# Performance work log

Measured on AMD Instinct MI355X. Metric: run time of the kernel, lower is better.

## Reference

```python
import jax, jax.numpy as jnp
import numpy as np
from jax import lax

ROUTE_SCALE = 1.0
TOPK = 2


def conv2d(x, w, stride=1, pad=1):
    # x: [B, Cin, H, W], w: [Cout, Cin, kh, kw]
    return lax.conv_general_dilated(
        x, w, window_strides=(stride, stride),
        padding=[(pad, pad), (pad, pad)],
        dimension_numbers=("NCHW", "OIHW", "NCHW"))


def setup_inputs() -> dict:
    key = jax.random.key(0)
    ks = jax.random.split(key, 6)
    B, Cin, Cout, H, W, E = 8, 32, 32, 256, 256, 8
    x = jax.random.normal(ks[0], (B, Cin, H, W), dtype=jnp.float32)
    gate_w = jax.random.normal(ks[1], (E, Cin, 3, 3), dtype=jnp.float32) * 0.05
    gate_bias = jnp.zeros((E,), dtype=jnp.float32)  # load-balance bias buffer (zero in eval)
    expert_w = jax.random.normal(ks[2], (E, Cout, Cin, 3, 3), dtype=jnp.float32) * 0.05
    expert_b = jax.random.normal(ks[3], (E, Cout), dtype=jnp.float32) * 0.05
    shared_w = jax.random.normal(ks[4], (Cout, Cin, 3, 3), dtype=jnp.float32) * 0.05
    shared_b = jax.random.normal(ks[5], (Cout,), dtype=jnp.float32) * 0.05
    return {"x": x, "gate_w": gate_w, "gate_bias": gate_bias,
            "expert_w": expert_w, "expert_b": expert_b,
            "shared_w": shared_w, "shared_b": shared_b}


def reference(x, gate_w, gate_bias, expert_w, expert_b, shared_w, shared_b):
    B, Cin, H, W = x.shape
    E, Cout = expert_w.shape[0], expert_w.shape[1]
    # ---- Gate: sigmoid(conv) -> per-pixel top-k over expert channel dim ----
    scores = jax.nn.sigmoid(conv2d(x, gate_w))                 # [B, E, H, W]
    biased = scores + gate_bias[None, :, None, None]
    st = jnp.moveaxis(scores, 1, -1)                            # [B, H, W, E]
    bt = jnp.moveaxis(biased, 1, -1)
    _, idx = lax.top_k(bt, TOPK)                                # [B, H, W, K]
    w = jnp.take_along_axis(st, idx, axis=-1)                   # gather raw scores
    w = jax.nn.softmax(w, axis=-1) * ROUTE_SCALE                # [B, H, W, K]
    # dense per-expert routing weight: sum_k w_k * onehot(idx_k)
    onehot = jax.nn.one_hot(idx, E, dtype=x.dtype)              # [B, H, W, K, E]
    dense = jnp.einsum('bhwk,bhwke->bhwe', w, onehot)           # [B, H, W, E]
    dense = jnp.moveaxis(dense, -1, 1)                          # [B, E, H, W]
    # ---- All expert convs as one stacked conv, masked accumulate ----
    ew = expert_w.reshape(E * Cout, Cin, 3, 3)
    eo = conv2d(x, ew) + expert_b.reshape(-1)[None, :, None, None]
    eo = eo.reshape(B, E, Cout, H, W)
    out = jnp.einsum('bechw,behw->bchw', eo, dense)
    # ---- Shared expert ----
    out = out + conv2d(x, shared_w) + shared_b[None, :, None, None]
    return out
```

## Files before the change

kernel.cpp:

```cpp
#include <hip/hip_runtime.h>

typedef __attribute__((ext_vector_type(8)))  short bf16x8;
typedef __attribute__((ext_vector_type(16))) float f32x16;

#define XIM (32*256*256)

__device__ __forceinline__ short f2bf(float f){
    unsigned int u = __builtin_bit_cast(unsigned int, f);
    u += 0x7fffu + ((u >> 16) & 1u);
    return (short)(u >> 16);
}
__device__ __forceinline__ float bf2f(short s){
    unsigned int u = ((unsigned int)(unsigned short)s) << 16;
    return __builtin_bit_cast(float, u);
}
__device__ __forceinline__ void glds16(const short* g, short* l){
    __builtin_amdgcn_global_load_lds(
        (const __attribute__((address_space(1))) unsigned int*)g,
        (__attribute__((address_space(3))) unsigned int*)l,
        16, 0, 0);
}

__global__ __launch_bounds__(256) void prep_weights(const float* __restrict__ ew,
                                                    const float* __restrict__ sw,
                                                    const float* __restrict__ ebv,
                                                    const float* __restrict__ sbv,
                                                    short* __restrict__ wt2){
    int i = blockIdx.x * 256 + threadIdx.x;
    if(i < 73728){
        int c7  = i & 7;
        int col = (i >> 3) & 31;
        int cio = (i >> 8) & 3;
        int rest = i >> 10;
        int tap = rest % 9;
        int es  = rest / 9;
        int ci  = cio*8 + c7;
        float v = ew[((es*32 + col)*32 + ci)*9 + tap] + sw[(col*32 + ci)*9 + tap];
        wt2[i] = f2bf(v);
    } else {
        int j = i - 73728, c = j >> 4, k = j & 15;
        float v = (k < 8) ? (ebv[k*32 + c] + sbv[c]) : 0.f;
        wt2[i] = f2bf(v);
    }
}

__global__ __launch_bounds__(256) void gate_kernel(const float* __restrict__ x,
                                                   const float* __restrict__ gw,
                                                   const float* __restrict__ gb,
                                                   short* __restrict__ route){
    __shared__ float xs[2][16][272];
    int raw = blockIdx.x;
    int wg  = (raw & 7)*128 + (raw >> 3);
    int b   = wg >> 7;
    int y0  = (wg & 127) * 2;
    int t   = threadIdx.x;
    int wv  = t >> 6, lane = t & 63;
    const float* xim = x + (size_t)b * XIM;

    if(t < 64){
        int bufi = t >> 5, s2 = (t >> 1) & 15;
        if(t & 1) xs[bufi][s2][260] = 0.f; else xs[bufi][s2][3] = 0.f;
    }

    float4 ld[4];
    auto LOAD = [&](int cc){
        #pragma unroll
        for(int sg=0; sg<4; ++sg){
            int seg = wv*4 + sg;
            int r4  = seg >> 2, cid = seg & 3;
            int ci  = cc*4 + cid;
            int yy  = y0 - 1 + r4;
            float4 v = make_float4(0.f,0.f,0.f,0.f);
            if(yy >= 0 && yy < 256)
                v = *(const float4*)(xim + ((size_t)ci*256 + yy)*256 + lane*4);
            ld[sg] = v;
        }
    };
    auto WRITE = [&](int bufi){
        #pragma unroll
        for(int sg=0; sg<4; ++sg){
            int seg = wv*4 + sg;
            *(float4*)(&xs[bufi][seg][4 + lane*4]) = ld[sg];
        }
    };

    float g[2][8];
    #pragma unroll
    for(int pr=0;pr<2;++pr)
        #pragma unroll
        for(int e=0;e<8;++e) g[pr][e] = 0.f;

    LOAD(0); WRITE(0);
    __syncthreads();
    for(int cc=0; cc<8; ++cc){
        if(cc < 7) LOAD(cc+1);
        const int bufi = cc & 1;
        #pragma unroll
        for(int cid=0; cid<4; ++cid){
            float sv[4][3];
            #pragma unroll
            for(int r4=0;r4<4;++r4){
                sv[r4][0] = xs[bufi][r4*4+cid][t+3];
                sv[r4][1] = xs[bufi][r4*4+cid][t+4];
                sv[r4][2] = xs[bufi][r4*4+cid][t+5];
            }
            const float* gwp = gw + (cc*4 + cid)*9;
            #pragma unroll
            for(int e=0;e<8;++e){
                #pragma unroll
                for(int kh=0;kh<3;++kh){
                    #pragma unroll
                    for(int kw=0;kw<3;++kw){
                        float wval = gwp[e*288 + kh*3 + kw];
                        g[0][e] = fmaf(sv[kh][kw],   wval, g[0][e]);
                        g[1][e] = fmaf(sv[kh+1][kw], wval, g[1][e]);
                    }
                }
            }
        }
        if(cc < 7) WRITE((cc+1)&1);
        __syncthreads();
    }

    #pragma unroll
    for(int pr=0; pr<2; ++pr){
        float v1b=-1e30f, v2b=-1e30f, v3b=-1e30f, r1=0.f, r2=0.f; int i1=-1, i2=-1;
        #pragma unroll
        for(int e=0;e<8;e++){
            float se = 1.f/(1.f + expf(-g[pr][e]));
            float be = se + gb[e];
            if(be > v1b){ v3b=v2b; v2b=v1b; r2=r1; i2=i1; v1b=be; r1=se; i1=e; }
            else if(be > v2b){ v3b=v2b; v2b=be; r2=se; i2=e; }
            else if(be > v3b){ v3b=be; }
        }
        if(v2b - v3b < 2e-5f){
            int y = y0 + pr;
            double gd[8];
            #pragma unroll
            for(int e=0;e<8;e++) gd[e] = 0.0;
            for(int ci=0; ci<32; ++ci){
                for(int kh=0; kh<3; ++kh){
                    int yy = y + kh - 1;
                    if(yy < 0 || yy >= 256) continue;
                    const float* xr = xim + ((size_t)ci*256 + yy)*256;
                    for(int kw=0; kw<3; ++kw){
                        int xx = t + kw - 1;
                        if(xx < 0 || xx >= 256) continue;
                        double xv = (double)xr[xx];
                        const float* gwp = gw + ci*9 + kh*3 + kw;
                        #pragma unroll
                        for(int e=0;e<8;e++) gd[e] += xv * (double)gwp[e*288];
                    }
                }
            }
            double b1=-1e30, b2=-1e30; double rr1=0.0, rr2=0.0; int j1=-1, j2=-1;
            #pragma unroll
            for(int e=0;e<8;e++){
                double sd = 1.0/(1.0 + exp(-gd[e]));
                double bd = sd + (double)gb[e];
                if(bd > b1){ b2=b1; rr2=rr1; j2=j1; b1=bd; rr1=sd; j1=e; }
                else if(bd > b2){ b2=bd; rr2=sd; j2=e; }
            }
            i1=j1; i2=j2; r1=(float)rr1; r2=(float)rr2;
        }
        float m  = fmaxf(r1, r2);
        float e1 = expf(r1-m), e2 = expf(r2-m);
        float inv = 1.f/(e1+e2);
        float w1 = e1*inv, w2 = e2*inv;
        bf16x8 ov;
        #pragma unroll
        for(int e=0;e<8;e++){
            float dv = (e==i1) ? w1 : ((e==i2) ? w2 : 0.f);
            ov[e] = f2bf(dv);
        }
        *(bf16x8*)(route + ((size_t)(b*256 + y0 + pr)*256 + t)*8) = ov;
    }
}

__global__ __launch_bounds__(512, 2) void moe_main(const float* __restrict__ x,
                                                   const short* __restrict__ wt2,
                                                   const short* __restrict__ route,
                                                   float* __restrict__ out){
    __shared__ __align__(16) short wlds[73728];
    __shared__ __align__(16) short xt[10*2*34*8];
    int raw = blockIdx.x;
    int wg  = (raw & 7)*256 + (raw >> 3);
    int b   = wg >> 8;
    int y0  = ((wg >> 3) & 31) * 8;
    int x0  = (wg & 7) * 32;
    int t   = threadIdx.x;
    int wv  = t >> 6, l = t & 63, col = l & 31, hi = l >> 5;

    #pragma unroll
    for(int j=0;j<18;++j){
        int c = wv + 8*j;
        glds16(wt2 + c*512 + l*8, wlds + c*512);
    }

    const float* xim = x + (size_t)b*XIM;
    int yy = y0 + wv;
    bf16x8 biasA = *(const bf16x8*)(wt2 + 73728 + col*16 + hi*8);
    bf16x8 rfrag = *(const bf16x8*)(route + ((size_t)(b*256 + yy)*256 + x0 + col)*8);

    bf16x8 Bf[3][2][3];
    #pragma unroll
    for(int hf=0; hf<2; ++hf){
        if(hf) __syncthreads();
        #pragma unroll
        for(int i=0;i<2;++i){
            int u = t + i*512;
            if(u < 640){
                int px = u & 31, rc = u >> 5;
                int row = rc >> 1, cic = rc & 1;
                int cib = hf*16 + cic*8;
                int ry = y0 - 1 + row, xx = x0 - 1 + px;
                bool ok = (ry>=0 && ry<256 && xx>=0 && xx<256);
                bf16x8 pk;
                #pragma unroll
                for(int j2=0;j2<8;++j2){
                    float v = ok ? xim[((size_t)(cib+j2)*256 + ry)*256 + xx] : 0.f;
                    pk[j2] = f2bf(v);
                }
                *(bf16x8*)(&xt[((row*2 + cic)*34 + px)*8]) = pk;
            }
        }
        if(t < 40){
            int pxh = 32 + (t & 1), rc = t >> 1;
            int row = rc >> 1, cic = rc & 1;
            int cib = hf*16 + cic*8;
            int ry = y0 - 1 + row, xx = x0 - 1 + pxh;
            bool ok = (ry>=0 && ry<256 && xx>=0 && xx<256);
            bf16x8 pk;
            #pragma unroll
            for(int j2=0;j2<8;++j2){
                float v = ok ? xim[((size_t)(cib+j2)*256 + ry)*256 + xx] : 0.f;
                pk[j2] = f2bf(v);
            }
            *(bf16x8*)(&xt[((row*2 + cic)*34 + pxh)*8]) = pk;
        }
        __syncthreads();
        #pragma unroll
        for(int kh=0;kh<3;++kh)
            #pragma unroll
            for(int kw=0;kw<3;++kw)
                Bf[kh][hf][kw] = *(const bf16x8*)(&xt[(((wv+kh)*2 + hi)*34 + col + kw)*8]);
    }

    f32x16 z = {};
    f32x16 oa = __builtin_amdgcn_mfma_f32_32x32x16_bf16(biasA, rfrag, z, 0,0,0);

    #pragma unroll
    for(int es=0; es<8; ++es){
        f32x16 acc = {};
        #pragma unroll
        for(int tap=0; tap<9; ++tap){
            const int kh = tap/3, kw = tap - kh*3;
            #pragma unroll
            for(int hf=0; hf<2; ++hf){
                bf16x8 a = *(const bf16x8*)(&wlds[(((es*9 + tap)*4 + hf*2 + hi)*32 + col)*8]);
                acc = __builtin_amdgcn_mfma_f32_32x32x16_bf16(a, Bf[kh][hf][kw], acc, 0,0,0);
            }
        }
        float d = bf2f(rfrag[es]);
        #pragma unroll
        for(int r=0;r<16;r++) oa[r] += d*acc[r];
    }

    float* ob = out + (size_t)b*XIM;
    #pragma unroll
    for(int r=0;r<16;r++){
        int c = hi*4 + (r&3) + 8*(r>>2);
        ob[((size_t)c*256 + yy)*256 + x0 + col] = oa[r];
    }
}

extern "C" void kernel_launch(void* const* d_in, const int* in_sizes, int n_in,
                              void* d_out, int out_size, void* d_ws, size_t ws_size,
                              hipStream_t stream){
    (void)in_sizes; (void)n_in; (void)out_size; (void)ws_size;
    const float* x   = (const float*)d_in[0];
    const float* gw  = (const float*)d_in[1];
    const float* gb  = (const float*)d_in[2];
    const float* ew  = (const float*)d_in[3];
    const float* ebv = (const float*)d_in[4];
    const float* sw  = (const float*)d_in[5];
    const float* sbv = (const float*)d_in[6];
    float* out = (float*)d_out;

    short* route = (short*)d_ws;
    short* wt2   = route + (size_t)8*256*256*8;

    prep_weights<<<dim3(290),  dim3(256), 0, stream>>>(ew, sw, ebv, sbv, wt2);
    gate_kernel <<<dim3(1024), dim3(256), 0, stream>>>(x, gw, gb, route);
    moe_main    <<<dim3(2048), dim3(512), 0, stream>>>(x, wt2, route, out);
}
```

Before: 220.2 us.

## Fuse gate conv into main MFMA kernel with fp16 and exact-route fixup pass

Removes the separate fp32 gate kernel and its route buffer. The gate conv now runs as extra fp16 MFMAs inside the main kernel, reusing the already-staged input tiles. All MFMAs switch from bf16 to fp16 for more mantissa precision. Pixels whose top-2 margin is ambiguous are appended to an atomic list, and two new kernels recompute their routing in double precision and rewrite their outputs in fp32. This trades a full gate pass and route traffic for an atomic counter, extra gate MFMAs, two small serial fixup kernels, and a hard cap on how many pixels can be fixed.

```diff
diff --git a/kernel.cpp b/kernel.cpp
--- a/kernel.cpp
+++ b/kernel.cpp
@@ -1,18 +1,14 @@
 #include <hip/hip_runtime.h>
 
-typedef __attribute__((ext_vector_type(8)))  short bf16x8;
+typedef __attribute__((ext_vector_type(8)))  _Float16 f16x8;
 typedef __attribute__((ext_vector_type(16))) float f32x16;
 
 #define XIM (32*256*256)
-
-__device__ __forceinline__ short f2bf(float f){
-    unsigned int u = __builtin_bit_cast(unsigned int, f);
-    u += 0x7fffu + ((u >> 16) & 1u);
-    return (short)(u >> 16);
-}
-__device__ __forceinline__ float bf2f(short s){
-    unsigned int u = ((unsigned int)(unsigned short)s) << 16;
-    return __builtin_bit_cast(float, u);
+#define MAXFIX 32768
+
+__device__ __forceinline__ short f2h(float f){
+    _Float16 h = (_Float16)f;
+    return __builtin_bit_cast(short, h);
 }
 __device__ __forceinline__ void glds16(const short* g, short* l){
     __builtin_amdgcn_global_load_lds(
@@ -25,8 +21,12 @@
                                                     const float* __restrict__ sw,
                                                     const float* __restrict__ ebv,
                                                     const float* __restrict__ sbv,
-                                                    short* __restrict__ wt2){
+                                                    const float* __restrict__ gw,
+                                                    short* __restrict__ wt2,
+                                                    short* __restrict__ gwA,
+                                                    int* __restrict__ cnt){
     int i = blockIdx.x * 256 + threadIdx.x;
+    if(i == 0) *cnt = 0;
     if(i < 73728){
         int c7  = i & 7;
         int col = (i >> 3) & 31;
@@ -36,151 +36,29 @@
         int es  = rest / 9;
         int ci  = cio*8 + c7;
         float v = ew[((es*32 + col)*32 + ci)*9 + tap] + sw[(col*32 + ci)*9 + tap];
-        wt2[i] = f2bf(v);
-    } else {
+        wt2[i] = f2h(v);
+    } else if(i < 74240){
         int j = i - 73728, c = j >> 4, k = j & 15;
         float v = (k < 8) ? (ebv[k*32 + c] + sbv[c]) : 0.f;
-        wt2[i] = f2bf(v);
-    }
-}
-
-__global__ __launch_bounds__(256) void gate_kernel(const float* __restrict__ x,
-                                                   const float* __restrict__ gw,
-                                                   const float* __restrict__ gb,
-                                                   short* __restrict__ route){
-    __shared__ float xs[2][16][272];
-    int raw = blockIdx.x;
-    int wg  = (raw & 7)*128 + (raw >> 3);
-    int b   = wg >> 7;
-    int y0  = (wg & 127) * 2;
-    int t   = threadIdx.x;
-    int wv  = t >> 6, lane = t & 63;
-    const float* xim = x + (size_t)b * XIM;
-
-    if(t < 64){
-        int bufi = t >> 5, s2 = (t >> 1) & 15;
-        if(t & 1) xs[bufi][s2][260] = 0.f; else xs[bufi][s2][3] = 0.f;
-    }
-
-    float4 ld[4];
-    auto LOAD = [&](int cc){
-        #pragma unroll
-        for(int sg=0; sg<4; ++sg){
-            int seg = wv*4 + sg;
-            int r4  = seg >> 2, cid = seg & 3;
-            int ci  = cc*4 + cid;
-            int yy  = y0 - 1 + r4;
-            float4 v = make_float4(0.f,0.f,0.f,0.f);
-            if(yy >= 0 && yy < 256)
-                v = *(const float4*)(xim + ((size_t)ci*256 + yy)*256 + lane*4);
-            ld[sg] = v;
-        }
-    };
-    auto WRITE = [&](int bufi){
-        #pragma unroll
-        for(int sg=0; sg<4; ++sg){
-            int seg = wv*4 + sg;
-            *(float4*)(&xs[bufi][seg][4 + lane*4]) = ld[sg];
-        }
-    };
-
-    float g[2][8];
-    #pragma unroll
-    for(int pr=0;pr<2;++pr)
-        #pragma unroll
-        for(int e=0;e<8;++e) g[pr][e] = 0.f;
-
-    LOAD(0); WRITE(0);
-    __syncthreads();
-    for(int cc=0; cc<8; ++cc){
-        if(cc < 7) LOAD(cc+1);
-        const int bufi = cc & 1;
-        #pragma unroll
-        for(int cid=0; cid<4; ++cid){
-            float sv[4][3];
-            #pragma unroll
-            for(int r4=0;r4<4;++r4){
-                sv[r4][0] = xs[bufi][r4*4+cid][t+3];
-                sv[r4][1] = xs[bufi][r4*4+cid][t+4];
-                sv[r4][2] = xs[bufi][r4*4+cid][t+5];
-            }
-            const float* gwp = gw + (cc*4 + cid)*9;
-            #pragma unroll
-            for(int e=0;e<8;++e){
-                #pragma unroll
-                for(int kh=0;kh<3;++kh){
-                    #pragma unroll
-                    for(int kw=0;kw<3;++kw){
-                        float wval = gwp[e*288 + kh*3 + kw];
-                        g[0][e] = fmaf(sv[kh][kw],   wval, g[0][e]);
-                        g[1][e] = fmaf(sv[kh+1][kw], wval, g[1][e]);
-                    }
-                }
-            }
-        }
-        if(cc < 7) WRITE((cc+1)&1);
-        __syncthreads();
-    }
-
-    #pragma unroll
-    for(int pr=0; pr<2; ++pr){
-        float v1b=-1e30f, v2b=-1e30f, v3b=-1e30f, r1=0.f, r2=0.f; int i1=-1, i2=-1;
-        #pragma unroll
-        for(int e=0;e<8;e++){
-            float se = 1.f/(1.f + expf(-g[pr][e]));
-            float be = se + gb[e];
-            if(be > v1b){ v3b=v2b; v2b=v1b; r2=r1; i2=i1; v1b=be; r1=se; i1=e; }
-            else if(be > v2b){ v3b=v2b; v2b=be; r2=se; i2=e; }
-            else if(be > v3b){ v3b=be; }
-        }
-        if(v2b - v3b < 2e-5f){
-            int y = y0 + pr;
-            double gd[8];
-            #pragma unroll
-            for(int e=0;e<8;e++) gd[e] = 0.0;
-            for(int ci=0; ci<32; ++ci){
-                for(int kh=0; kh<3; ++kh){
-                    int yy = y + kh - 1;
-                    if(yy < 0 || yy >= 256) continue;
-                    const float* xr = xim + ((size_t)ci*256 + yy)*256;
-                    for(int kw=0; kw<3; ++kw){
-                        int xx = t + kw - 1;
-                        if(xx < 0 || xx >= 256) continue;
-                        double xv = (double)xr[xx];
-                        const float* gwp = gw + ci*9 + kh*3 + kw;
-                        #pragma unroll
-                        for(int e=0;e<8;e++) gd[e] += xv * (double)gwp[e*288];
-                    }
-                }
-            }
-            double b1=-1e30, b2=-1e30; double rr1=0.0, rr2=0.0; int j1=-1, j2=-1;
-            #pragma unroll
-            for(int e=0;e<8;e++){
-                double sd = 1.0/(1.0 + exp(-gd[e]));
-                double bd = sd + (double)gb[e];
-                if(bd > b1){ b2=b1; rr2=rr1; j2=j1; b1=bd; rr1=sd; j1=e; }
-                else if(bd > b2){ b2=bd; rr2=sd; j2=e; }
-            }
-            i1=j1; i2=j2; r1=(float)rr1; r2=(float)rr2;
-        }
-        float m  = fmaxf(r1, r2);
-        float e1 = expf(r1-m), e2 = expf(r2-m);
-        float inv = 1.f/(e1+e2);
-        float w1 = e1*inv, w2 = e2*inv;
-        bf16x8 ov;
-        #pragma unroll
-        for(int e=0;e<8;e++){
-            float dv = (e==i1) ? w1 : ((e==i2) ? w2 : 0.f);
-            ov[e] = f2bf(dv);
-        }
-        *(bf16x8*)(route + ((size_t)(b*256 + y0 + pr)*256 + t)*8) = ov;
+        wt2[i] = f2h(v);
+    } else {
+        int i2 = i - 74240;
+        int c7  = i2 & 7;
+        int row = (i2 >> 3) & 31;
+        int cio = (i2 >> 8) & 3;
+        int tap = i2 >> 10;
+        float v = (row < 8) ? gw[row*288 + (cio*8 + c7)*9 + tap] : 0.f;
+        gwA[i2] = f2h(v);
     }
 }
 
 __global__ __launch_bounds__(512, 2) void moe_main(const float* __restrict__ x,
                                                    const short* __restrict__ wt2,
-                                                   const short* __restrict__ route,
-                                                   float* __restrict__ out){
+                                                   const short* __restrict__ gwA,
+                                                   const float* __restrict__ gb,
+                                                   float* __restrict__ out,
+                                                   int* __restrict__ cnt,
+                                                   int* __restrict__ fixlist){
     __shared__ __align__(16) short wlds[73728];
     __shared__ __align__(16) short xt[10*2*34*8];
     int raw = blockIdx.x;
@@ -199,10 +77,9 @@
 
     const float* xim = x + (size_t)b*XIM;
     int yy = y0 + wv;
-    bf16x8 biasA = *(const bf16x8*)(wt2 + 73728 + col*16 + hi*8);
-    bf16x8 rfrag = *(const bf16x8*)(route + ((size_t)(b*256 + yy)*256 + x0 + col)*8);
-
-    bf16x8 Bf[3][2][3];
+    f16x8 biasA = *(const f16x8*)(wt2 + 73728 + col*16 + hi*8);
+
+    f16x8 Bf[3][2][3];
     #pragma unroll
     for(int hf=0; hf<2; ++hf){
         if(hf) __syncthreads();
@@ -215,13 +92,13 @@
                 int cib = hf*16 + cic*8;
                 int ry = y0 - 1 + row, xx = x0 - 1 + px;
                 bool ok = (ry>=0 && ry<256 && xx>=0 && xx<256);
-                bf16x8 pk;
+                f16x8 pk;
                 #pragma unroll
                 for(int j2=0;j2<8;++j2){
                     float v = ok ? xim[((size_t)(cib+j2)*256 + ry)*256 + xx] : 0.f;
-                    pk[j2] = f2bf(v);
+                    pk[j2] = (_Float16)v;
                 }
-                *(bf16x8*)(&xt[((row*2 + cic)*34 + px)*8]) = pk;
+                *(f16x8*)(&xt[((row*2 + cic)*34 + px)*8]) = pk;
             }
         }
         if(t < 40){
@@ -230,24 +107,66 @@
             int cib = hf*16 + cic*8;
             int ry = y0 - 1 + row, xx = x0 - 1 + pxh;
             bool ok = (ry>=0 && ry<256 && xx>=0 && xx<256);
-            bf16x8 pk;
+            f16x8 pk;
             #pragma unroll
             for(int j2=0;j2<8;++j2){
                 float v = ok ? xim[((size_t)(cib+j2)*256 + ry)*256 + xx] : 0.f;
-                pk[j2] = f2bf(v);
-            }
-            *(bf16x8*)(&xt[((row*2 + cic)*34 + pxh)*8]) = pk;
+                pk[j2] = (_Float16)v;
+            }
+            *(f16x8*)(&xt[((row*2 + cic)*34 + pxh)*8]) = pk;
         }
         __syncthreads();
         #pragma unroll
         for(int kh=0;kh<3;++kh)
             #pragma unroll
             for(int kw=0;kw<3;++kw)
-                Bf[kh][hf][kw] = *(const bf16x8*)(&xt[(((wv+kh)*2 + hi)*34 + col + kw)*8]);
+                Bf[kh][hf][kw] = *(const f16x8*)(&xt[(((wv+kh)*2 + hi)*34 + col + kw)*8]);
+    }
+
+    f32x16 ga = {};
+    #pragma unroll
+    for(int tap=0; tap<9; ++tap){
+        const int kh = tap/3, kw = tap - kh*3;
+        #pragma unroll
+        for(int hf=0; hf<2; ++hf){
+            f16x8 a = *(const f16x8*)(gwA + ((tap*4 + hf*2 + hi)*32 + col)*8);
+            ga = __builtin_amdgcn_mfma_f32_32x32x16_f16(a, Bf[kh][hf][kw], ga, 0,0,0);
+        }
+    }
+    float gsc[8];
+    #pragma unroll
+    for(int j=0;j<4;++j){
+        float own = ga[j];
+        float prt = __shfl_xor(own, 32);
+        gsc[j]   = hi ? prt : own;
+        gsc[4+j] = hi ? own : prt;
+    }
+    float v1b=-1e30f, v2b=-1e30f, v3b=-1e30f, r1=0.f, r2=0.f; int i1=-1, i2=-1;
+    #pragma unroll
+    for(int e=0;e<8;e++){
+        float se = 1.f/(1.f + expf(-gsc[e]));
+        float be = se + gb[e];
+        if(be > v1b){ v3b=v2b; v2b=v1b; r2=r1; i2=i1; v1b=be; r1=se; i1=e; }
+        else if(be > v2b){ v3b=v2b; v2b=be; r2=se; i2=e; }
+        else if(be > v3b){ v3b=be; }
+    }
+    if(hi == 0 && (v2b - v3b < 1e-3f)){
+        int slot = atomicAdd(cnt, 1);
+        if(slot < MAXFIX) fixlist[slot] = (b << 16) | (yy << 8) | (x0 + col);
+    }
+    float m  = fmaxf(r1, r2);
+    float e1 = expf(r1-m), e2 = expf(r2-m);
+    float inv = 1.f/(e1+e2);
+    float w1 = e1*inv, w2 = e2*inv;
+    f16x8 rfrag;
+    #pragma unroll
+    for(int e=0;e<8;e++){
+        float dv = (e==i1) ? w1 : ((e==i2) ? w2 : 0.f);
+        rfrag[e] = (_Float16)dv;
     }
 
     f32x16 z = {};
-    f32x16 oa = __builtin_amdgcn_mfma_f32_32x32x16_bf16(biasA, rfrag, z, 0,0,0);
+    f32x16 oa = __builtin_amdgcn_mfma_f32_32x32x16_f16(biasA, rfrag, z, 0,0,0);
 
     #pragma unroll
     for(int es=0; es<8; ++es){
@@ -257,11 +176,11 @@
             const int kh = tap/3, kw = tap - kh*3;
             #pragma unroll
             for(int hf=0; hf<2; ++hf){
-                bf16x8 a = *(const bf16x8*)(&wlds[(((es*9 + tap)*4 + hf*2 + hi)*32 + col)*8]);
-                acc = __builtin_amdgcn_mfma_f32_32x32x16_bf16(a, Bf[kh][hf][kw], acc, 0,0,0);
-            }
-        }
-        float d = bf2f(rfrag[es]);
+                f16x8 a = *(const f16x8*)(&wlds[(((es*9 + tap)*4 + hf*2 + hi)*32 + col)*8]);
+                acc = __builtin_amdgcn_mfma_f32_32x32x16_f16(a, Bf[kh][hf][kw], acc, 0,0,0);
+            }
+        }
+        float d = (es==i1) ? w1 : ((es==i2) ? w2 : 0.f);
         #pragma unroll
         for(int r=0;r<16;r++) oa[r] += d*acc[r];
     }
@@ -271,6 +190,91 @@
     for(int r=0;r<16;r++){
         int c = hi*4 + (r&3) + 8*(r>>2);
         ob[((size_t)c*256 + yy)*256 + x0 + col] = oa[r];
+    }
+}
+
+__global__ __launch_bounds__(256) void fixup_route(const float* __restrict__ x,
+                                                   const float* __restrict__ gw,
+                                                   const float* __restrict__ gb,
+                                                   const int* __restrict__ cnt,
+                                                   const int* __restrict__ fixlist,
+                                                   int4* __restrict__ fxroute){
+    int n = *cnt; if(n > MAXFIX) n = MAXFIX;
+    for(int idx = blockIdx.x*256 + threadIdx.x; idx < n; idx += 32*256){
+        int pix = fixlist[idx];
+        int b  = pix >> 16, y = (pix >> 8) & 255, xx = pix & 255;
+        const float* xim = x + (size_t)b*XIM;
+        double gd[8];
+        #pragma unroll
+        for(int e=0;e<8;e++) gd[e] = 0.0;
+        for(int ci=0; ci<32; ++ci){
+            for(int kh=0; kh<3; ++kh){
+                int yy = y + kh - 1;
+                if(yy < 0 || yy >= 256) continue;
+                const float* xr = xim + ((size_t)ci*256 + yy)*256;
+                for(int kw=0; kw<3; ++kw){
+                    int xc = xx + kw - 1;
+                    if(xc < 0 || xc >= 256) continue;
+                    double xv = (double)xr[xc];
+                    #pragma unroll
+                    for(int e=0;e<8;e++) gd[e] += xv * (double)gw[e*288 + ci*9 + kh*3 + kw];
+                }
+            }
+        }
+        double b1=-1e30, b2=-1e30; double rr1=0.0, rr2=0.0; int j1=-1, j2=-1;
+        #pragma unroll
+        for(int e=0;e<8;e++){
+            double sd = 1.0/(1.0 + exp(-gd[e]));
+            double bd = sd + (double)gb[e];
+            if(bd > b1){ b2=b1; rr2=rr1; j2=j1; b1=bd; rr1=sd; j1=e; }
+            else if(bd > b2){ b2=bd; rr2=sd; j2=e; }
+        }
+        float r1 = (float)rr1, r2 = (float)rr2;
+        float m  = fmaxf(r1, r2);
+        float e1 = expf(r1-m), e2 = expf(r2-m);
+        float inv = 1.f/(e1+e2);
+        fxroute[idx] = make_int4(j1, j2, __float_as_int(e1*inv), __float_as_int(e2*inv));
+    }
+}
+
+__global__ __launch_bounds__(256) void fixup_out(const float* __restrict__ x,
+                                                 const float* __restrict__ ew,
+                                                 const float* __restrict__ sw,
+                                                 const float* __restrict__ ebv,
+                                                 const float* __restrict__ sbv,
+                                                 const int* __restrict__ cnt,
+                                                 const int* __restrict__ fixlist,
+                                                 const int4* __restrict__ fxroute,
+                                                 float* __restrict__ out){
+    int n = *cnt; if(n > MAXFIX) n = MAXFIX;
+    int total = n * 32;
+    for(int u = blockIdx.x*256 + threadIdx.x; u < total; u += 256*256){
+        int idx = u >> 5, c = u & 31;
+        int pix = fixlist[idx];
+        int b  = pix >> 16, y = (pix >> 8) & 255, xx = pix & 255;
+        int4 fr = fxroute[idx];
+        int i1 = fr.x, i2 = fr.y;
+        float w1 = __int_as_float(fr.z), w2 = __int_as_float(fr.w);
+        float acc = w1*ebv[i1*32 + c] + w2*ebv[i2*32 + c] + sbv[c];
+        const float* xim = x + (size_t)b*XIM;
+        const float* e1w = ew + ((size_t)(i1*32 + c))*288;
+        const float* e2w = ew + ((size_t)(i2*32 + c))*288;
+        const float* shw = sw + (size_t)c*288;
+        for(int ci=0; ci<32; ++ci){
+            for(int kh=0; kh<3; ++kh){
+                int yy = y + kh - 1;
+                if(yy < 0 || yy >= 256) continue;
+                const float* xr = xim + ((size_t)ci*256 + yy)*256;
+                for(int kw=0; kw<3; ++kw){
+                    int xc = xx + kw - 1;
+                    if(xc < 0 || xc >= 256) continue;
+                    int wi = ci*9 + kh*3 + kw;
+                    float wv = w1*e1w[wi] + w2*e2w[wi] + shw[wi];
+                    acc = fmaf(xr[xc], wv, acc);
+                }
+            }
+        }
+        out[(size_t)b*XIM + ((size_t)c*256 + y)*256 + xx] = acc;
     }
 }
 
@@ -287,10 +291,14 @@
     const float* sbv = (const float*)d_in[6];
     float* out = (float*)d_out;
 
-    short* route = (short*)d_ws;
-    short* wt2   = route + (size_t)8*256*256*8;
-
-    prep_weights<<<dim3(290),  dim3(256), 0, stream>>>(ew, sw, ebv, sbv, wt2);
-    gate_kernel <<<dim3(1024), dim3(256), 0, stream>>>(x, gw, gb, route);
-    moe_main    <<<dim3(2048), dim3(512), 0, stream>>>(x, wt2, route, out);
-}
+    short* wt2   = (short*)d_ws;
+    short* gwA   = wt2 + 74240;
+    int*   cnt   = (int*)((char*)d_ws + 166912);
+    int*   fixlist = cnt + 4;
+    int4*  fxroute = (int4*)((char*)d_ws + 298000);
+
+    prep_weights<<<dim3(326),  dim3(256), 0, stream>>>(ew, sw, ebv, sbv, gw, wt2, gwA, cnt);
+    moe_main    <<<dim3(2048), dim3(512), 0, stream>>>(x, wt2, gwA, gb, out, cnt, fixlist);
+    fixup_route <<<dim3(32),   dim3(256), 0, stream>>>(x, gw, gb, cnt, fixlist, fxroute);
+    fixup_out   <<<dim3(256),  dim3(256), 0, stream>>>(x, ew, sw, ebv, sbv, cnt, fixlist, fxroute, out);
+}
```

Measured after the change: 636.4 us. 189% more time.
